# Kernel optimization log

Measured on AMD Instinct MI355X. Metric: run time of the kernel, lower is better.

## Reference

```python
import jax, jax.numpy as jnp
import numpy as np

N = 256
WINDOW = 16
HORIZON = 12
STEPS_PER_WEEK = 4
DT = 1.0 / STEPS_PER_WEEK


def setup_inputs() -> dict:
    key = jax.random.key(0)
    ks = jax.random.split(key, 8)
    B = 512
    x_hist = jax.random.uniform(ks[0], (B, WINDOW, N), dtype=jnp.float32)
    cnn_feat = jax.random.normal(ks[1], (B, 64), dtype=jnp.float32)
    s = 0.02  # small init scale to keep sigmoids/softmax well-behaved
    W1 = jax.random.normal(ks[2], (WINDOW * N, 128), dtype=jnp.float32) * s
    b1 = jnp.zeros((128,), jnp.float32)
    W2 = jax.random.normal(ks[3], (128, 4 * N), dtype=jnp.float32) * s
    b2 = jnp.zeros((4 * N,), jnp.float32)
    M1 = jax.random.normal(ks[4], (64, 128), dtype=jnp.float32) * s
    mb1 = jnp.zeros((128,), jnp.float32)
    M2 = jax.random.normal(ks[5], (128, N * N), dtype=jnp.float32) * s
    mb2 = jnp.zeros((N * N,), jnp.float32)
    return {"x_hist": x_hist, "cnn_feat": cnn_feat, "W1": W1, "b1": b1,
            "W2": W2, "b2": b2, "M1": M1, "mb1": mb1, "M2": M2, "mb2": mb2}


def reference(x_hist, cnn_feat, W1, b1, W2, b2, M1, mb1, M2, mb2):
    B, T, n = x_hist.shape
    # param_net: Linear -> ReLU -> Linear
    h = jax.nn.relu(x_hist.reshape(B, -1) @ W1 + b1)
    params = h @ W2 + b2  # (B, 4N)
    beta = jax.nn.sigmoid(params[:, :n]) * 3.0
    sigma = jax.nn.sigmoid(params[:, n:2 * n]) * 1.0
    gamma = jax.nn.sigmoid(params[:, 2 * n:3 * n]) * 1.0
    e0_ratio = jax.nn.sigmoid(params[:, 3 * n:]) * 5.0
    # mobility_net -> row-softmax mobility matrix Pi (B, N, N)
    hm = jax.nn.relu(cnn_feat @ M1 + mb1)
    Pi = jax.nn.softmax((hm @ M2 + mb2).reshape(B, n, n), axis=-1)

    I0 = jnp.maximum(x_hist[:, -1], 1e-6)
    E0 = I0 * e0_ratio
    S0 = jnp.maximum(1.0 - E0 - I0, 0.01)

    def get_grads(S, E, I):
        # bmm(I[:,None,:], Pi).squeeze(1) == einsum bn,bnm->bm
        force = jnp.einsum('bn,bnm->bm', I, Pi)
        new_inf = beta * S * force
        return -new_inf, new_inf - sigma * E, sigma * E - gamma * I

    def week_step(carry, _):
        S, E, I = carry
        for _ in range(STEPS_PER_WEEK):
            dS1, dE1, dI1 = get_grads(S, E, I)
            dS2, dE2, dI2 = get_grads(S + 0.5 * DT * dS1, E + 0.5 * DT * dE1, I + 0.5 * DT * dI1)
            dS3, dE3, dI3 = get_grads(S + 0.5 * DT * dS2, E + 0.5 * DT * dE2, I + 0.5 * DT * dI2)
            dS4, dE4, dI4 = get_grads(S + DT * dS3, E + DT * dE3, I + DT * dI3)
            S = jnp.clip(S + DT / 6.0 * (dS1 + 2 * dS2 + 2 * dS3 + dS4), 0.0, 1.0)
            E = jnp.clip(E + DT / 6.0 * (dE1 + 2 * dE2 + 2 * dE3 + dE4), 0.0, 1.0)
            I = jnp.clip(I + DT / 6.0 * (dI1 + 2 * dI2 + 2 * dI3 + dI4), 0.0, 1.0)
        return (S, E, I), (I, E)

    _, (I_s, E_s) = jax.lax.scan(week_step, (S0, E0, I0), None, length=HORIZON)
    I_sim = jnp.swapaxes(I_s, 0, 1)  # (B, horizon, N)
    E_sim = jnp.swapaxes(E_s, 0, 1)
    return (I_sim, E_sim, beta.mean(0), sigma.mean(0), gamma.mean(0), Pi.mean(0))
```

## Files before the change

kernel.cpp:

```cpp
#include <hip/hip_runtime.h>
#include <hip/hip_bf16.h>
#include <stdint.h>
#include <stddef.h>

typedef _Float16 half2_t __attribute__((ext_vector_type(2)));
typedef _Float16 f16x8 __attribute__((ext_vector_type(8)));
typedef float f32x4 __attribute__((ext_vector_type(4)));

__global__ __launch_bounds__(256, 2) void k_paramnet1(
    const float* __restrict__ X, const float* __restrict__ W1,
    float* __restrict__ hpart) {
  const int ks = blockIdx.x;
  const int b0 = blockIdx.y * 32;
  const int t = threadIdx.x;

  __shared__ float sw[128 * 128];
  __shared__ float sx[32 * 128];

  {
    const float4* src = (const float4*)(W1 + (size_t)ks * 16384);
    float4* dst = (float4*)sw;
#pragma unroll
    for (int i = 0; i < 16; ++i) dst[t + i * 256] = src[t + i * 256];
  }
  {
    const int r = t >> 3, c = t & 7;
    const float4* srcr = (const float4*)(X + (size_t)(b0 + r) * 4096 + ks * 128);
    float4* dstr = (float4*)(sx + r * 128);
#pragma unroll
    for (int i = 0; i < 4; ++i) dstr[c + i * 8] = srcr[c + i * 8];
  }
  __syncthreads();

  const int j = t & 127;
  const int rh = t >> 7;

  float acc[16];
#pragma unroll
  for (int i = 0; i < 16; ++i) acc[i] = 0.f;

  for (int k4 = 0; k4 < 32; ++k4) {
    const float w0 = sw[(k4 * 4 + 0) * 128 + j];
    const float w1v = sw[(k4 * 4 + 1) * 128 + j];
    const float w2 = sw[(k4 * 4 + 2) * 128 + j];
    const float w3 = sw[(k4 * 4 + 3) * 128 + j];
#pragma unroll
    for (int i = 0; i < 16; ++i) {
      const float4 xv = *(const float4*)(sx + (rh + 2 * i) * 128 + k4 * 4);
      acc[i] = fmaf(xv.x, w0,
               fmaf(xv.y, w1v,
               fmaf(xv.z, w2,
               fmaf(xv.w, w3, acc[i]))));
    }
  }
#pragma unroll
  for (int i = 0; i < 16; ++i) {
    const int row = b0 + rh + 2 * i;
    hpart[((size_t)ks * 512 + row) * 128 + j] = acc[i];
  }
}

__global__ __launch_bounds__(256) void k_paramnet2(
    const float* __restrict__ hpart, const float* __restrict__ b1,
    float* __restrict__ h) {
  const int idx = blockIdx.x * 256 + threadIdx.x;
  float s = b1[idx & 127];
#pragma unroll
  for (int ks = 0; ks < 32; ++ks) s += hpart[(size_t)ks * 65536 + idx];
  h[idx] = fmaxf(s, 0.f);
}

__global__ __launch_bounds__(256) void k_params_state(
    const float* __restrict__ h, const float* __restrict__ W2,
    const float* __restrict__ b2, const float* __restrict__ X,
    float* __restrict__ betaW, float* __restrict__ sigmaW,
    float* __restrict__ gammaW, float* __restrict__ S0W,
    float* __restrict__ E0W, float* __restrict__ I0W,
    float* __restrict__ stats) {
  const int b0 = blockIdx.x * 2;
  const int t = threadIdx.x;
  const float* h0 = h + (size_t)b0 * 128;
  const float* h1 = h0 + 128;
  float a00 = b2[t], a01 = b2[256 + t], a02 = b2[512 + t], a03 = b2[768 + t];
  float a10 = a00, a11 = a01, a12 = a02, a13 = a03;
#pragma unroll 2
  for (int k = 0; k < 128; ++k) {
    const float* wr = W2 + (size_t)k * 1024;
    const float w0 = wr[t], w1 = wr[256 + t], w2 = wr[512 + t], w3 = wr[768 + t];
    const float hv0 = h0[k], hv1 = h1[k];
    a00 = fmaf(hv0, w0, a00); a01 = fmaf(hv0, w1, a01);
    a02 = fmaf(hv0, w2, a02); a03 = fmaf(hv0, w3, a03);
    a10 = fmaf(hv1, w0, a10); a11 = fmaf(hv1, w1, a11);
    a12 = fmaf(hv1, w2, a12); a13 = fmaf(hv1, w3, a13);
  }
  float bsum = 0.f, ssum = 0.f, gsum = 0.f;
#pragma unroll
  for (int j = 0; j < 2; ++j) {
    const float p0 = j ? a10 : a00, p1 = j ? a11 : a01;
    const float p2 = j ? a12 : a02, p3 = j ? a13 : a03;
    const float beta = 3.f / (1.f + __expf(-p0));
    const float sig  = 1.f / (1.f + __expf(-p1));
    const float gam  = 1.f / (1.f + __expf(-p2));
    const float e0r  = 5.f / (1.f + __expf(-p3));
    const int base = (b0 + j) * 256 + t;
    const float I0 = fmaxf(X[(size_t)(b0 + j) * 4096 + 15 * 256 + t], 1e-6f);
    const float E0 = I0 * e0r;
    const float S0 = fmaxf(1.f - E0 - I0, 0.01f);
    betaW[base] = beta; sigmaW[base] = sig; gammaW[base] = gam;
    S0W[base] = S0; E0W[base] = E0; I0W[base] = I0;
    bsum += beta; ssum += sig; gsum += gam;
  }
  atomicAdd(stats + t, bsum);
  atomicAdd(stats + 256 + t, ssum);
  atomicAdd(stats + 512 + t, gsum);
}

__global__ __launch_bounds__(256) void k_cvtM2(
    const float* __restrict__ M2, _Float16* __restrict__ M2T,
    const float* __restrict__ cnn, const float* __restrict__ M1,
    const float* __restrict__ mb1, _Float16* __restrict__ hmf) {
  const int n = blockIdx.x, t = threadIdx.x;

  {
    const int b = 2 * n + (t >> 7);
    const int j = t & 127;
    const float* cr = cnn + b * 64;
    float a = mb1[j];
#pragma unroll
    for (int k = 0; k < 64; ++k) a = fmaf(cr[k], M1[k * 128 + j], a);
    hmf[n * 256 + t] = (_Float16)fmaxf(a, 0.f);
  }

  __shared__ _Float16 sm[128 * 256];
  const float* src = M2 + (size_t)n * 256 + t;
#pragma unroll 8
  for (int k = 0; k < 128; ++k)
    sm[k * 256 + t] = (_Float16)src[(size_t)k * 65536];
  __syncthreads();
  half2_t col[64];
#pragma unroll 16
  for (int k2 = 0; k2 < 64; ++k2)
    col[k2] = half2_t{sm[(2 * k2) * 256 + t], sm[(2 * k2 + 1) * 256 + t]};
  uint4* dst = (uint4*)(M2T + ((size_t)n * 256 + t) * 128);
  const uint4* s4 = (const uint4*)col;
#pragma unroll
  for (int i = 0; i < 16; ++i) dst[i] = s4[i];
}

__global__ __launch_bounds__(512, 2) void k_mobility2(
    const _Float16* __restrict__ hmf, const _Float16* __restrict__ M2T,
    const float* __restrict__ mb2, _Float16* __restrict__ PiF,
    float* __restrict__ pimpart) {
  const int n = blockIdx.x;
  const int pass = blockIdx.y;
  const int tid = threadIdx.x;
  const int wave = tid >> 6;
  const int lane = tid & 63;
  const int q = lane >> 4;
  const int c = lane & 15;

  __shared__ _Float16 sm[8][16 * 256];

  const _Float16* Bbase = M2T + (size_t)n * 32768 + (size_t)c * 128 + q * 8;
  const float* mbp = mb2 + n * 256 + c;

  const int bt0 = wave * 4 + pass * 2;
  f32x4 C0[16], C1[16];
#pragma unroll
  for (int nb = 0; nb < 16; ++nb) {
    const float mbv = mbp[nb * 16];
    C0[nb] = f32x4{mbv, mbv, mbv, mbv};
    C1[nb] = C0[nb];
  }
  const _Float16* A0 = hmf + (size_t)(bt0 * 16 + c) * 128 + q * 8;
  const _Float16* A1 = A0 + 16 * 128;
#pragma unroll
  for (int ks = 0; ks < 4; ++ks) {
    const f16x8 Af0 = *(const f16x8*)(A0 + ks * 32);
    const f16x8 Af1 = *(const f16x8*)(A1 + ks * 32);
#pragma unroll
    for (int nb = 0; nb < 16; ++nb) {
      const f16x8 Bf = *(const f16x8*)(Bbase + nb * 2048 + ks * 32);
      C0[nb] = __builtin_amdgcn_mfma_f32_16x16x32_f16(Af0, Bf, C0[nb], 0, 0, 0);
      C1[nb] = __builtin_amdgcn_mfma_f32_16x16x32_f16(Af1, Bf, C1[nb], 0, 0, 0);
    }
  }

  float colsum[16];
#pragma unroll
  for (int nb = 0; nb < 16; ++nb) colsum[nb] = 0.f;

#pragma unroll
  for (int half = 0; half < 2; ++half) {
    f32x4* C = half ? C1 : C0;
    const int bt = bt0 + half;
    float mx[4], sum[4];
#pragma unroll
    for (int r = 0; r < 4; ++r) mx[r] = C[0][r];
#pragma unroll
    for (int nb = 1; nb < 16; ++nb)
#pragma unroll
      for (int r = 0; r < 4; ++r) mx[r] = fmaxf(mx[r], C[nb][r]);
#pragma unroll
    for (int r = 0; r < 4; ++r) {
      mx[r] = fmaxf(mx[r], __shfl_xor(mx[r], 1, 16));
      mx[r] = fmaxf(mx[r], __shfl_xor(mx[r], 2, 16));
      mx[r] = fmaxf(mx[r], __shfl_xor(mx[r], 4, 16));
      mx[r] = fmaxf(mx[r], __shfl_xor(mx[r], 8, 16));
      sum[r] = 0.f;
    }
#pragma unroll
    for (int nb = 0; nb < 16; ++nb)
#pragma unroll
      for (int r = 0; r < 4; ++r) {
        const float e = __expf(C[nb][r] - mx[r]);
        C[nb][r] = e;
        sum[r] += e;
      }
#pragma unroll
    for (int r = 0; r < 4; ++r) {
      sum[r] += __shfl_xor(sum[r], 1, 16);
      sum[r] += __shfl_xor(sum[r], 2, 16);
      sum[r] += __shfl_xor(sum[r], 4, 16);
      sum[r] += __shfl_xor(sum[r], 8, 16);
      sum[r] = 1.f / sum[r];
    }
    _Float16* slot = sm[wave];
#pragma unroll
    for (int nb = 0; nb < 16; ++nb) {
#pragma unroll
      for (int r = 0; r < 4; ++r) {
        const float v = C[nb][r] * sum[r];
        colsum[nb] += v;
        slot[(q * 4 + r) * 256 + nb * 16 + c] = (_Float16)v;
      }
    }
    const int l2 = lane & 31, rh = lane >> 5;
    _Float16* Pg = PiF + ((size_t)(bt * 16) * 256 + n) * 256;
#pragma unroll
    for (int i = 0; i < 8; ++i) {
      const int row = i * 2 + rh;
      const uint4 v = *(const uint4*)(slot + row * 256 + l2 * 8);
      *(uint4*)(Pg + (size_t)row * 65536 + l2 * 8) = v;
    }
  }
#pragma unroll
  for (int nb = 0; nb < 16; ++nb) {
    colsum[nb] += __shfl_xor(colsum[nb], 16);
    colsum[nb] += __shfl_xor(colsum[nb], 32);
  }
  if (lane < 16) {
    float* pp = pimpart + n * 256 + lane;
#pragma unroll
    for (int nb = 0; nb < 16; ++nb) atomicAdd(pp + nb * 16, colsum[nb]);
  }
}

__global__ __launch_bounds__(256, 2) void k_sim_part(
    const _Float16* __restrict__ PiF, const float* __restrict__ betaW,
    const float* __restrict__ sigmaW, const float* __restrict__ gammaW,
    float* __restrict__ SW, float* __restrict__ EW, float* __restrict__ IW,
    const float* __restrict__ stats, const float* __restrict__ pimpart,
    float* __restrict__ out, int wk0, int nwk, int do_finalize) {
  const int b = blockIdx.x;
  const int tid = threadIdx.x;

  if (do_finalize) {
    const int g = b * 256 + tid;
    if (g < 66304) {
      const float inv = 1.f / 512.f;
      if (g < 768) out[3145728 + g] = stats[g] * inv;
      else out[3146496 + (g - 768)] = pimpart[g - 768] * inv;
    }
  }

  const int w = tid >> 6, lane = tid & 63;
  const int q = lane >> 4, c = lane & 15;
  const int mown = (4 * w + q) * 16 + c;

  __shared__ __align__(16) _Float16 Ib[2][256];

  f16x8 Bf[4][8];
  {
    const _Float16* P = PiF + (size_t)b * 65536 + (size_t)(q * 8) * 256 + c;
#pragma unroll
    for (int i = 0; i < 4; ++i) {
#pragma unroll
      for (int t = 0; t < 8; ++t) {
        const _Float16* src = P + (size_t)(t * 32) * 256 + (4 * w + i) * 16;
        f16x8 v;
#pragma unroll
        for (int j = 0; j < 8; ++j) v[j] = src[(size_t)j * 256];
        Bf[i][t] = v;
      }
    }
  }

  const int base = b * 256 + mown;
  const float bet = betaW[base], sig = sigmaW[base], gam = gammaW[base];
  float S = SW[base], E = EW[base], I = IW[base];

  int p = 0;
  auto grads = [&](float Ss, float Es, float Is, float& dS, float& dE, float& dI) {
    Ib[p][mown] = (_Float16)Is;
    __syncthreads();
    const f16x8* ia = (const f16x8*)Ib[p];
    p ^= 1;
    f32x4 C[4];
#pragma unroll
    for (int i = 0; i < 4; ++i) C[i] = f32x4{0.f, 0.f, 0.f, 0.f};
#pragma unroll
    for (int t = 0; t < 8; ++t) {
      const f16x8 A = ia[t * 4 + q];
#pragma unroll
      for (int i = 0; i < 4; ++i)
        C[i] = __builtin_amdgcn_mfma_f32_16x16x32_f16(A, Bf[i][t], C[i], 0, 0, 0);
    }
    const float force = (q & 2) ? ((q & 1) ? C[3][0] : C[2][0])
                                : ((q & 1) ? C[1][0] : C[0][0]);
    const float ninf = bet * Ss * force;
    const float sE = sig * Es;
    dS = -ninf;
    dE = ninf - sE;
    dI = sE - gam * Is;
  };

  float* outI = out + (size_t)b * (12 * 256) + mown;
  float* outE = outI + 1572864;
  const float c6 = 0.25f / 6.f;

  for (int wk = wk0; wk < wk0 + nwk; ++wk) {
    for (int st = 0; st < 4; ++st) {
      float d1S, d1E, d1I, d2S, d2E, d2I, d3S, d3E, d3I, d4S, d4E, d4I;
      grads(S, E, I, d1S, d1E, d1I);
      grads(S + 0.125f * d1S, E + 0.125f * d1E, I + 0.125f * d1I, d2S, d2E, d2I);
      grads(S + 0.125f * d2S, E + 0.125f * d2E, I + 0.125f * d2I, d3S, d3E, d3I);
      grads(S + 0.25f * d3S, E + 0.25f * d3E, I + 0.25f * d3I, d4S, d4E, d4I);
      S = fminf(fmaxf(S + c6 * (d1S + 2.f * d2S + 2.f * d3S + d4S), 0.f), 1.f);
      E = fminf(fmaxf(E + c6 * (d1E + 2.f * d2E + 2.f * d3E + d4E), 0.f), 1.f);
      I = fminf(fmaxf(I + c6 * (d1I + 2.f * d2I + 2.f * d3I + d4I), 0.f), 1.f);
    }
    outI[wk * 256] = I;
    outE[wk * 256] = E;
  }

  SW[base] = S; EW[base] = E; IW[base] = I;
}

extern "C" void kernel_launch(void* const* d_in, const int* in_sizes, int n_in,
                              void* d_out, int out_size, void* d_ws, size_t ws_size,
                              hipStream_t stream) {
  const float* x_hist = (const float*)d_in[0];
  const float* cnn    = (const float*)d_in[1];
  const float* W1     = (const float*)d_in[2];
  const float* b1     = (const float*)d_in[3];
  const float* W2     = (const float*)d_in[4];
  const float* b2     = (const float*)d_in[5];
  const float* M1     = (const float*)d_in[6];
  const float* mb1    = (const float*)d_in[7];
  const float* M2     = (const float*)d_in[8];
  const float* mb2    = (const float*)d_in[9];
  float* out = (float*)d_out;

  char* w = (char*)d_ws;
  _Float16* M2T     = (_Float16*)(w + 0);
  _Float16* hmf     = (_Float16*)(w + 16777216);
  float*    betaW   = (float*)(w + 16908288);
  float*    sigmaW  = (float*)(w + 17432576);
  float*    gammaW  = (float*)(w + 17956864);
  float*    S0W     = (float*)(w + 18481152);
  float*    E0W     = (float*)(w + 19005440);
  float*    I0W     = (float*)(w + 19529728);
  float*    pimpart = (float*)(w + 20054016);
  float*    stats   = (float*)(w + 20316160);
  _Float16* PiF     = (_Float16*)(w + 20320256);
  float*    hpart   = (float*)(w + 20320256);
  float*    h       = (float*)(w + 28708864);

  hipMemsetAsync(pimpart, 0, 266240, stream);
  k_paramnet1<<<dim3(32, 16), 256, 0, stream>>>(x_hist, W1, hpart);
  k_paramnet2<<<256, 256, 0, stream>>>(hpart, b1, h);
  k_params_state<<<256, 256, 0, stream>>>(h, W2, b2, x_hist, betaW, sigmaW,
                                          gammaW, S0W, E0W, I0W, stats);
  k_cvtM2<<<256, 256, 0, stream>>>(M2, M2T, cnn, M1, mb1, hmf);
  k_mobility2<<<dim3(256, 2), 512, 0, stream>>>(hmf, M2T, mb2, PiF, pimpart);
  k_sim_part<<<512, 256, 0, stream>>>(PiF, betaW, sigmaW, gammaW, S0W, E0W,
                                      I0W, stats, pimpart, out, 0, 6, 1);
  k_sim_part<<<512, 256, 0, stream>>>(PiF, betaW, sigmaW, gammaW, S0W, E0W,
                                      I0W, stats, pimpart, out, 6, 6, 0);
}
```

Measured before the change: 382.5 us.

## Split params kernel per batch, vectorize M2 loads, split simulation into four launches

Three unrelated changes. The params kernel now handles one batch row per block over 512 blocks instead of two rows per block, which gives more parallelism but reads W2 twice as often and doubles the atomic adds. The M2 transpose/convert kernel loads float4 row-contiguous chunks instead of strided scalar loads, aiming for better coalescing. The simulation is split into four launches of 3 weeks each instead of two of 6, which adds launch overhead and state round-trips, possibly to shorten individual kernels or reduce register pressure.

```diff
diff --git a/kernel.cpp b/kernel.cpp
--- a/kernel.cpp
+++ b/kernel.cpp
@@ -77,42 +77,32 @@
     float* __restrict__ gammaW, float* __restrict__ S0W,
     float* __restrict__ E0W, float* __restrict__ I0W,
     float* __restrict__ stats) {
-  const int b0 = blockIdx.x * 2;
+  const int b = blockIdx.x;
   const int t = threadIdx.x;
-  const float* h0 = h + (size_t)b0 * 128;
-  const float* h1 = h0 + 128;
-  float a00 = b2[t], a01 = b2[256 + t], a02 = b2[512 + t], a03 = b2[768 + t];
-  float a10 = a00, a11 = a01, a12 = a02, a13 = a03;
-#pragma unroll 2
+  const float* h0 = h + (size_t)b * 128;
+  float a0 = b2[t], a1 = b2[256 + t], a2 = b2[512 + t], a3 = b2[768 + t];
+#pragma unroll 4
   for (int k = 0; k < 128; ++k) {
     const float* wr = W2 + (size_t)k * 1024;
-    const float w0 = wr[t], w1 = wr[256 + t], w2 = wr[512 + t], w3 = wr[768 + t];
-    const float hv0 = h0[k], hv1 = h1[k];
-    a00 = fmaf(hv0, w0, a00); a01 = fmaf(hv0, w1, a01);
-    a02 = fmaf(hv0, w2, a02); a03 = fmaf(hv0, w3, a03);
-    a10 = fmaf(hv1, w0, a10); a11 = fmaf(hv1, w1, a11);
-    a12 = fmaf(hv1, w2, a12); a13 = fmaf(hv1, w3, a13);
-  }
-  float bsum = 0.f, ssum = 0.f, gsum = 0.f;
-#pragma unroll
-  for (int j = 0; j < 2; ++j) {
-    const float p0 = j ? a10 : a00, p1 = j ? a11 : a01;
-    const float p2 = j ? a12 : a02, p3 = j ? a13 : a03;
-    const float beta = 3.f / (1.f + __expf(-p0));
-    const float sig  = 1.f / (1.f + __expf(-p1));
-    const float gam  = 1.f / (1.f + __expf(-p2));
-    const float e0r  = 5.f / (1.f + __expf(-p3));
-    const int base = (b0 + j) * 256 + t;
-    const float I0 = fmaxf(X[(size_t)(b0 + j) * 4096 + 15 * 256 + t], 1e-6f);
-    const float E0 = I0 * e0r;
-    const float S0 = fmaxf(1.f - E0 - I0, 0.01f);
-    betaW[base] = beta; sigmaW[base] = sig; gammaW[base] = gam;
-    S0W[base] = S0; E0W[base] = E0; I0W[base] = I0;
-    bsum += beta; ssum += sig; gsum += gam;
-  }
-  atomicAdd(stats + t, bsum);
-  atomicAdd(stats + 256 + t, ssum);
-  atomicAdd(stats + 512 + t, gsum);
+    const float hv = h0[k];
+    a0 = fmaf(hv, wr[t], a0);
+    a1 = fmaf(hv, wr[256 + t], a1);
+    a2 = fmaf(hv, wr[512 + t], a2);
+    a3 = fmaf(hv, wr[768 + t], a3);
+  }
+  const float beta = 3.f / (1.f + __expf(-a0));
+  const float sig  = 1.f / (1.f + __expf(-a1));
+  const float gam  = 1.f / (1.f + __expf(-a2));
+  const float e0r  = 5.f / (1.f + __expf(-a3));
+  const int base = b * 256 + t;
+  const float I0 = fmaxf(X[(size_t)b * 4096 + 15 * 256 + t], 1e-6f);
+  const float E0 = I0 * e0r;
+  const float S0 = fmaxf(1.f - E0 - I0, 0.01f);
+  betaW[base] = beta; sigmaW[base] = sig; gammaW[base] = gam;
+  S0W[base] = S0; E0W[base] = E0; I0W[base] = I0;
+  atomicAdd(stats + t, beta);
+  atomicAdd(stats + 256 + t, sig);
+  atomicAdd(stats + 512 + t, gam);
 }
 
 __global__ __launch_bounds__(256) void k_cvtM2(
@@ -132,10 +122,19 @@
   }
 
   __shared__ _Float16 sm[128 * 256];
-  const float* src = M2 + (size_t)n * 256 + t;
+  {
+    const int kk = t >> 6, c4 = t & 63;
 #pragma unroll 8
-  for (int k = 0; k < 128; ++k)
-    sm[k * 256 + t] = (_Float16)src[(size_t)k * 65536];
+    for (int i = 0; i < 32; ++i) {
+      const int row = i * 4 + kk;
+      const float4 v =
+          *(const float4*)(M2 + (size_t)row * 65536 + n * 256 + c4 * 4);
+      sm[row * 256 + c4 * 4 + 0] = (_Float16)v.x;
+      sm[row * 256 + c4 * 4 + 1] = (_Float16)v.y;
+      sm[row * 256 + c4 * 4 + 2] = (_Float16)v.z;
+      sm[row * 256 + c4 * 4 + 3] = (_Float16)v.w;
+    }
+  }
   __syncthreads();
   half2_t col[64];
 #pragma unroll 16
@@ -380,12 +379,16 @@
   hipMemsetAsync(pimpart, 0, 266240, stream);
   k_paramnet1<<<dim3(32, 16), 256, 0, stream>>>(x_hist, W1, hpart);
   k_paramnet2<<<256, 256, 0, stream>>>(hpart, b1, h);
-  k_params_state<<<256, 256, 0, stream>>>(h, W2, b2, x_hist, betaW, sigmaW,
+  k_params_state<<<512, 256, 0, stream>>>(h, W2, b2, x_hist, betaW, sigmaW,
                                           gammaW, S0W, E0W, I0W, stats);
   k_cvtM2<<<256, 256, 0, stream>>>(M2, M2T, cnn, M1, mb1, hmf);
   k_mobility2<<<dim3(256, 2), 512, 0, stream>>>(hmf, M2T, mb2, PiF, pimpart);
   k_sim_part<<<512, 256, 0, stream>>>(PiF, betaW, sigmaW, gammaW, S0W, E0W,
-                                      I0W, stats, pimpart, out, 0, 6, 1);
+                                      I0W, stats, pimpart, out, 0, 3, 1);
   k_sim_part<<<512, 256, 0, stream>>>(PiF, betaW, sigmaW, gammaW, S0W, E0W,
-                                      I0W, stats, pimpart, out, 6, 6, 0);
-}
+                                      I0W, stats, pimpart, out, 3, 3, 0);
+  k_sim_part<<<512, 256, 0, stream>>>(PiF, betaW, sigmaW, gammaW, S0W, E0W,
+                                      I0W, stats, pimpart, out, 6, 3, 0);
+  k_sim_part<<<512, 256, 0, stream>>>(PiF, betaW, sigmaW, gammaW, S0W, E0W,
+                                      I0W, stats, pimpart, out, 9, 3, 0);
+}
```

Measured after the change: 411.6 us. 7.6% more time.
